# Performance work log

Hardware: AMD Instinct MI355X
Metric: run time of the kernel (lower is better)

Reference implementation:

```python
import jax, jax.numpy as jnp
import numpy as np

N, E = 100000, 1600000
FEATS, HIDDEN, CLASSES, DEPTH = 512, 64, 16, 10
EMB_DIM = 1 + int(np.log2(HIDDEN))   # 7
ADJ_H = 4 + EMB_DIM                  # 11
DIFF = 0.9


def setup_inputs() -> dict:
    key = jax.random.key(0)
    ks = jax.random.split(key, 8)
    return {
        "x": jax.random.normal(ks[0], (N, FEATS), jnp.float32),
        "edges": jax.random.randint(ks[1], (2, E), 0, N, jnp.int32),
        "W_dim": jax.random.normal(ks[2], (FEATS, HIDDEN), jnp.float32) / np.sqrt(FEATS),
        "b_dim": jnp.zeros((HIDDEN,), jnp.float32),
        "emb": jax.random.normal(ks[3], (HIDDEN, EMB_DIM), jnp.float32),
        "W_a1": jax.random.normal(ks[4], (2 + EMB_DIM, ADJ_H), jnp.float32) / np.sqrt(2 + EMB_DIM),
        "b_a1": jnp.zeros((ADJ_H,), jnp.float32),
        "W_a2": jax.random.normal(ks[5], (ADJ_H, 1), jnp.float32) / np.sqrt(ADJ_H),
        "b_a2": jnp.zeros((1,), jnp.float32),
        "W_cls": jax.random.normal(ks[6], (HIDDEN, CLASSES), jnp.float32) / np.sqrt(HIDDEN),
        "b_cls": jnp.zeros((CLASSES,), jnp.float32),
    }


def reference(x, edges, W_dim, b_dim, emb, W_a1, b_a1, W_a2, b_a2, W_cls, b_cls):
    n = x.shape[0]
    src, dst = edges[0], edges[1]
    # symmetric-normalized sparse aggregation (GCN-style GraphConv, cached norm)
    deg = jax.ops.segment_sum(jnp.ones(src.shape[0], x.dtype), dst, num_segments=n)
    dinv = jnp.where(deg > 0, jax.lax.rsqrt(jnp.maximum(deg, 1.0)), 0.0)
    wnorm = dinv[src] * dinv[dst]  # [E]

    def conv(h):  # [n, H] -> [n, H]
        return jax.ops.segment_sum(h[src] * wnorm[:, None], dst, num_segments=n)

    h = x @ W_dim + b_dim        # [n, HIDDEN]
    h0 = h
    for _ in range(DEPTH):       # personalized-PageRank-style diffusion
        h = conv(h) * DIFF + (1.0 - DIFF) * h0

    hdim = h.shape[1]
    xt = h.T.reshape(-1, 1)      # [HIDDEN*n, 1]
    h0t = h0.T.reshape(-1, 1)
    # class_indicator built after reshape(-1,1): num_classes = 1 -> all-zero indices
    e = jnp.broadcast_to(emb[0], (xt.shape[0], emb.shape[1]))  # [HIDDEN*n, EMB_DIM]
    f = jnp.concatenate([xt, h0t, e], axis=1)                  # [HIDDEN*n, 9]
    f = jax.nn.leaky_relu(f @ W_a1 + b_a1, negative_slope=0.01)
    f = (f @ W_a2 + b_a2) * 0.5                                # [HIDDEN*n, 1]
    h = f.reshape(hdim, n).T                                   # [n, HIDDEN]
    # dropout: eval mode -> no-op
    h0 = h
    for _ in range(DEPTH):
        h = conv(h) * DIFF + (1.0 - DIFF) * h0
    return h @ W_cls + b_cls     # [n, CLASSES]
```

## Files before the change

kernel.cpp:

```cpp
#include <hip/hip_runtime.h>
#include <hip/hip_bf16.h>
#include <hip/hip_fp16.h>
#include <stdint.h>

#define FEATS   512
#define HIDDEN  64
#define CLASSES 16
#define EMB_DIM 7
#define ADJ_H   11
#define DEPTH   10

typedef __hip_bfloat16 bf16;
typedef __attribute__((ext_vector_type(8))) short short8;
typedef __attribute__((ext_vector_type(4))) float f32x4;

__device__ __forceinline__ float b2f(bf16 v) { return __bfloat162float(v); }

__global__ void k_detect(const unsigned short* __restrict__ xs, int* __restrict__ flag) {
    __shared__ int cnt;
    if (threadIdx.x == 0) cnt = 0;
    __syncthreads();
    int c = 0;
    for (int i = threadIdx.x; i < 4096; i += 256) {
        unsigned e = (xs[i] >> 7) & 0xFFu;
        if (e >= 134u) c++;
    }
    atomicAdd(&cnt, c);
    __syncthreads();
    if (threadIdx.x == 0) *flag = (cnt < 64) ? 1 : 0;
}

__global__ __launch_bounds__(256) void k_deg(const int* __restrict__ edges,
                                             int* __restrict__ deg, int E) {
    int e = blockIdx.x * 256 + threadIdx.x;
    if (e < E) atomicAdd(&deg[edges[E + e]], 1);
}

__global__ __launch_bounds__(256) void k_scan1(const int* __restrict__ deg,
                                               int* __restrict__ offs,
                                               int* __restrict__ bsum, int n) {
    __shared__ int ts[256];
    int t = threadIdx.x;
    int base = blockIdx.x * 1024 + t * 4;
    int v0 = (base + 0 < n) ? deg[base + 0] : 0;
    int v1 = (base + 1 < n) ? deg[base + 1] : 0;
    int v2 = (base + 2 < n) ? deg[base + 2] : 0;
    int v3 = (base + 3 < n) ? deg[base + 3] : 0;
    int tsum = v0 + v1 + v2 + v3;
    ts[t] = tsum;
    __syncthreads();
    for (int d = 1; d < 256; d <<= 1) {
        int add = (t >= d) ? ts[t - d] : 0;
        __syncthreads();
        ts[t] += add;
        __syncthreads();
    }
    int excl = ts[t] - tsum;
    if (base + 0 < n) offs[base + 0] = excl;
    if (base + 1 < n) offs[base + 1] = excl + v0;
    if (base + 2 < n) offs[base + 2] = excl + v0 + v1;
    if (base + 3 < n) offs[base + 3] = excl + v0 + v1 + v2;
    if (t == 255) bsum[blockIdx.x] = ts[255];
}

__global__ void k_scan2(const int* __restrict__ bsum, int* __restrict__ bpref,
                        int* __restrict__ offs, int nb, int n) {
    if (threadIdx.x == 0 && blockIdx.x == 0) {
        int run = 0;
        for (int i = 0; i < nb; ++i) { bpref[i] = run; run += bsum[i]; }
        offs[n] = run;
    }
}

__global__ __launch_bounds__(256) void k_scan3(int* __restrict__ offs,
                                               const int* __restrict__ bpref, int n) {
    int i = blockIdx.x * 256 + threadIdx.x;
    if (i < n) offs[i] += bpref[i >> 10];
}

__global__ __launch_bounds__(256) void k_fill(const int* __restrict__ edges,
                                              const int* __restrict__ offs,
                                              int* __restrict__ cursor,
                                              const int* __restrict__ deg,
                                              unsigned* __restrict__ ew, int E) {
    int e = blockIdx.x * 256 + threadIdx.x;
    if (e < E) {
        int src = edges[e];
        int dst = edges[E + e];
        int pos = offs[dst] + atomicAdd(&cursor[dst], 1);
        int ds = deg[src], dd = deg[dst];
        float w = (ds > 0 ? rsqrtf((float)ds) : 0.f) * (dd > 0 ? rsqrtf((float)dd) : 0.f);
        int w15 = (int)(w * 16384.0f + 0.5f);
        if (w15 > 32767) w15 = 32767;
        ew[pos] = ((unsigned)src << 15) | (unsigned)w15;
    }
}

__global__ void k_mlpconst(const void* __restrict__ emb, const void* __restrict__ W_a1,
                           const void* __restrict__ b_a1, const void* __restrict__ W_a2,
                           const void* __restrict__ b_a2, const int* __restrict__ flag,
                           float* __restrict__ C) {
    int isbf = *flag;
    auto g = [&](const void* p, int i) -> float {
        return isbf ? b2f(((const bf16*)p)[i]) : ((const float*)p)[i];
    };
    int j = threadIdx.x;
    if (j < ADJ_H) {
        float c = g(b_a1, j);
        for (int k = 0; k < EMB_DIM; ++k)
            c += g(emb, k) * g(W_a1, (2 + k) * ADJ_H + j);
        C[j]      = c;
        C[11 + j] = g(W_a1, 0 * ADJ_H + j);
        C[22 + j] = g(W_a1, 1 * ADJ_H + j);
        C[33 + j] = g(W_a2, j);
    }
    if (j == 0) C[44] = g(b_a2, 0);
}

__global__ __launch_bounds__(256) void k_gemm_mfma(const void* __restrict__ xraw,
                                                   const int* __restrict__ flag,
                                                   const void* __restrict__ Wraw,
                                                   const void* __restrict__ braw,
                                                   __half* __restrict__ out, int n) {
    __shared__ short Wt[64 * 520];
    int t = threadIdx.x;
    int isbf = *flag;
    if (isbf) {
        const unsigned short* wr = (const unsigned short*)Wraw;
        for (int e = t; e < FEATS * HIDDEN; e += 256)
            Wt[(e & 63) * 520 + (e >> 6)] = (short)wr[e];
    } else {
        const float* wr = (const float*)Wraw;
        for (int e = t; e < FEATS * HIDDEN; e += 256)
            Wt[(e & 63) * 520 + (e >> 6)] = (short)(__float_as_uint(wr[e]) >> 16);
    }
    __syncthreads();

    int wv = t >> 6;
    int lane = t & 63;
    int quad = lane >> 4, l16 = lane & 15;
    int rowbase = blockIdx.x * 256 + wv * 64;

    f32x4 acc[4][4];
    #pragma unroll
    for (int a = 0; a < 4; ++a)
        #pragma unroll
        for (int b = 0; b < 4; ++b)
            acc[a][b] = (f32x4){0.f, 0.f, 0.f, 0.f};

    if (isbf) {
        const short* x = (const short*)xraw;
        for (int ks = 0; ks < 16; ++ks) {
            short8 bfr[4];
            #pragma unroll
            for (int nt = 0; nt < 4; ++nt)
                bfr[nt] = *(const short8*)&Wt[(nt * 16 + l16) * 520 + ks * 32 + quad * 8];
            #pragma unroll
            for (int rt = 0; rt < 4; ++rt) {
                int arow = rowbase + rt * 16 + l16;
                if (arow >= n) arow = n - 1;
                short8 a = *(const short8*)(x + (size_t)arow * FEATS + ks * 32 + quad * 8);
                #pragma unroll
                for (int nt = 0; nt < 4; ++nt)
                    acc[rt][nt] = __builtin_amdgcn_mfma_f32_16x16x32_bf16(a, bfr[nt], acc[rt][nt], 0, 0, 0);
            }
        }
    } else {
        const float* x = (const float*)xraw;
        for (int ks = 0; ks < 16; ++ks) {
            short8 bfr[4];
            #pragma unroll
            for (int nt = 0; nt < 4; ++nt)
                bfr[nt] = *(const short8*)&Wt[(nt * 16 + l16) * 520 + ks * 32 + quad * 8];
            #pragma unroll
            for (int rt = 0; rt < 4; ++rt) {
                int arow = rowbase + rt * 16 + l16;
                if (arow >= n) arow = n - 1;
                const float* ap = x + (size_t)arow * FEATS + ks * 32 + quad * 8;
                short8 a;
                #pragma unroll
                for (int j = 0; j < 8; ++j)
                    a[j] = (short)(__float_as_uint(ap[j]) >> 16);
                #pragma unroll
                for (int nt = 0; nt < 4; ++nt)
                    acc[rt][nt] = __builtin_amdgcn_mfma_f32_16x16x32_bf16(a, bfr[nt], acc[rt][nt], 0, 0, 0);
            }
        }
    }

    float bias[4];
    #pragma unroll
    for (int nt = 0; nt < 4; ++nt)
        bias[nt] = isbf ? b2f(((const bf16*)braw)[nt * 16 + l16])
                        : ((const float*)braw)[nt * 16 + l16];

    #pragma unroll
    for (int rt = 0; rt < 4; ++rt)
        #pragma unroll
        for (int nt = 0; nt < 4; ++nt) {
            #pragma unroll
            for (int r = 0; r < 4; ++r) {
                int grow = rowbase + rt * 16 + quad * 4 + r;
                if (grow < n)
                    out[(size_t)grow * HIDDEN + nt * 16 + l16] =
                        __float2half(acc[rt][nt][r] + bias[nt]);
            }
        }
}

__global__ __launch_bounds__(256) void k_conv(const int* __restrict__ offs,
                                              const unsigned* __restrict__ ew,
                                              const __half* __restrict__ hin,
                                              const __half* __restrict__ h0,
                                              __half* __restrict__ hout, int n) {
    int wv = (blockIdx.x * 256 + threadIdx.x) >> 6;
    int nA = wv * 2;
    if (nA >= n) return;
    int nB = nA + 1;
    bool hasB = (nB < n);
    int lane = threadIdx.x & 63;
    int eg = lane >> 3;
    int li = lane & 7;
    int sA = offs[nA], eA = offs[nA + 1];
    int sB = hasB ? offs[nB] : 0;
    int eB = hasB ? offs[nB + 1] : 0;

    float4 a0 = make_float4(0.f,0.f,0.f,0.f), a1 = make_float4(0.f,0.f,0.f,0.f);
    float4 b0 = make_float4(0.f,0.f,0.f,0.f), b1 = make_float4(0.f,0.f,0.f,0.f);

    int pA = sA + eg, pB = sB + eg;
    while (pA < eA || pB < eB) {
        bool vA = pA < eA, vB = pB < eB;
        unsigned uA = 0, uB = 0;
        uint4 rA = make_uint4(0,0,0,0), rB = make_uint4(0,0,0,0);
        if (vA) {
            uA = ew[pA];
            rA = *(const uint4*)(hin + (size_t)(uA >> 15) * HIDDEN + li * 8);
        }
        if (vB) {
            uB = ew[pB];
            rB = *(const uint4*)(hin + (size_t)(uB >> 15) * HIDDEN + li * 8);
        }
        if (vA) {
            float w = (float)(uA & 0x7FFFu) * (1.0f / 16384.0f);
            float2 f0 = __half22float2(*(__half2*)&rA.x);
            float2 f1 = __half22float2(*(__half2*)&rA.y);
            float2 f2 = __half22float2(*(__half2*)&rA.z);
            float2 f3 = __half22float2(*(__half2*)&rA.w);
            a0.x += w*f0.x; a0.y += w*f0.y; a0.z += w*f1.x; a0.w += w*f1.y;
            a1.x += w*f2.x; a1.y += w*f2.y; a1.z += w*f3.x; a1.w += w*f3.y;
            pA += 8;
        }
        if (vB) {
            float w = (float)(uB & 0x7FFFu) * (1.0f / 16384.0f);
            float2 f0 = __half22float2(*(__half2*)&rB.x);
            float2 f1 = __half22float2(*(__half2*)&rB.y);
            float2 f2 = __half22float2(*(__half2*)&rB.z);
            float2 f3 = __half22float2(*(__half2*)&rB.w);
            b0.x += w*f0.x; b0.y += w*f0.y; b0.z += w*f1.x; b0.w += w*f1.y;
            b1.x += w*f2.x; b1.y += w*f2.y; b1.z += w*f3.x; b1.w += w*f3.y;
            pB += 8;
        }
    }

    #pragma unroll
    for (int d = 8; d <= 32; d <<= 1) {
        a0.x += __shfl_xor(a0.x, d); a0.y += __shfl_xor(a0.y, d);
        a0.z += __shfl_xor(a0.z, d); a0.w += __shfl_xor(a0.w, d);
        a1.x += __shfl_xor(a1.x, d); a1.y += __shfl_xor(a1.y, d);
        a1.z += __shfl_xor(a1.z, d); a1.w += __shfl_xor(a1.w, d);
        b0.x += __shfl_xor(b0.x, d); b0.y += __shfl_xor(b0.y, d);
        b0.z += __shfl_xor(b0.z, d); b0.w += __shfl_xor(b0.w, d);
        b1.x += __shfl_xor(b1.x, d); b1.y += __shfl_xor(b1.y, d);
        b1.z += __shfl_xor(b1.z, d); b1.w += __shfl_xor(b1.w, d);
    }

    if (eg < 2 && (eg == 0 || hasB)) {
        int node = (eg == 0) ? nA : nB;
        float4 c0 = (eg == 0) ? a0 : b0;
        float4 c1 = (eg == 0) ? a1 : b1;
        size_t o = (size_t)node * HIDDEN + li * 8;
        uint4 hv = *(const uint4*)(h0 + o);
        float2 g0 = __half22float2(*(__half2*)&hv.x);
        float2 g1 = __half22float2(*(__half2*)&hv.y);
        float2 g2 = __half22float2(*(__half2*)&hv.z);
        float2 g3 = __half22float2(*(__half2*)&hv.w);
        __half2 o0 = __floats2half2_rn(0.9f*c0.x + 0.1f*g0.x, 0.9f*c0.y + 0.1f*g0.y);
        __half2 o1 = __floats2half2_rn(0.9f*c0.z + 0.1f*g1.x, 0.9f*c0.w + 0.1f*g1.y);
        __half2 o2 = __floats2half2_rn(0.9f*c1.x + 0.1f*g2.x, 0.9f*c1.y + 0.1f*g2.y);
        __half2 o3 = __floats2half2_rn(0.9f*c1.z + 0.1f*g3.x, 0.9f*c1.w + 0.1f*g3.y);
        uint4 ov;
        ov.x = *(unsigned*)&o0; ov.y = *(unsigned*)&o1;
        ov.z = *(unsigned*)&o2; ov.w = *(unsigned*)&o3;
        *(uint4*)(hout + o) = ov;
    }
}

__global__ __launch_bounds__(256) void k_mlp(__half* __restrict__ h0io,
                                             const __half* __restrict__ hc,
                                             const float* __restrict__ C, int total2) {
    int i = blockIdx.x * 256 + threadIdx.x;
    if (i >= total2) return;
    float2 hv  = __half22float2(((const __half2*)hc)[i]);
    float2 h0v = __half22float2(((const __half2*)h0io)[i]);
    float sx = C[44], sy = C[44];
    #pragma unroll
    for (int j = 0; j < ADJ_H; ++j) {
        float bj = C[j], wh = C[11 + j], w0 = C[22 + j], wo = C[33 + j];
        float zx = bj + hv.x * wh + h0v.x * w0;
        float zy = bj + hv.y * wh + h0v.y * w0;
        zx = (zx > 0.f) ? zx : 0.01f * zx;
        zy = (zy > 0.f) ? zy : 0.01f * zy;
        sx += zx * wo;
        sy += zy * wo;
    }
    ((__half2*)h0io)[i] = __floats2half2_rn(0.5f * sx, 0.5f * sy);
}

__global__ __launch_bounds__(256) void k_cls(const __half* __restrict__ h,
                                             const void* __restrict__ Wcraw,
                                             const void* __restrict__ bcraw,
                                             void* __restrict__ outraw,
                                             const int* __restrict__ flag, int n) {
    __shared__ float hs[64][65];
    __shared__ float ws[64 * 16];
    __shared__ float bs[16];
    int t = threadIdx.x;
    int base = blockIdx.x * 64;
    int isbf = *flag;
    for (int it = 0; it < 16; ++it) {
        int e = it * 256 + t;
        int rr = e >> 6, cc = e & 63;
        int g = base + rr;
        hs[rr][cc] = (g < n) ? __half2float(h[(size_t)g * HIDDEN + cc]) : 0.f;
    }
    for (int it = 0; it < 4; ++it) {
        int e = it * 256 + t;
        ws[e] = isbf ? b2f(((const bf16*)Wcraw)[e]) : ((const float*)Wcraw)[e];
    }
    if (t < 16) bs[t] = isbf ? b2f(((const bf16*)bcraw)[t]) : ((const float*)bcraw)[t];
    __syncthreads();
    for (int q = 0; q < 4; ++q) {
        int e = q * 256 + t;
        int node = e >> 4, cls = e & 15;
        float acc = bs[cls];
        #pragma unroll 8
        for (int k = 0; k < HIDDEN; ++k)
            acc += hs[node][k] * ws[k * 16 + cls];
        int g = base + node;
        if (g < n) {
            size_t oi = (size_t)g * CLASSES + cls;
            if (isbf) ((bf16*)outraw)[oi] = __float2bfloat16(acc);
            else      ((float*)outraw)[oi] = acc;
        }
    }
}

extern "C" void kernel_launch(void* const* d_in, const int* in_sizes, int n_in,
                              void* d_out, int out_size, void* d_ws, size_t ws_size,
                              hipStream_t stream) {
    const void* x     = d_in[0];
    const int*  edges = (const int*)d_in[1];
    const void* W_dim = d_in[2];
    const void* b_dim = d_in[3];
    const void* emb   = d_in[4];
    const void* W_a1  = d_in[5];
    const void* b_a1  = d_in[6];
    const void* W_a2  = d_in[7];
    const void* b_a2  = d_in[8];
    const void* Wcls  = d_in[9];
    const void* bcls  = d_in[10];

    const int n = in_sizes[0] / FEATS;
    const int E = in_sizes[1] / 2;

    char* w = (char*)d_ws;
    size_t off = 0;
    auto alloc = [&](size_t bytes) -> void* {
        void* p = w + off;
        off = (off + bytes + 255) & ~(size_t)255;
        return p;
    };
    int*      deg    = (int*)     alloc((size_t)n * 4);
    int*      cursor = (int*)     alloc((size_t)n * 4);
    int*      offs   = (int*)     alloc((size_t)(n + 1) * 4);
    int*      bsum   = (int*)     alloc(4096 * 4);
    int*      bpref  = (int*)     alloc(4096 * 4);
    unsigned* ew     = (unsigned*)alloc((size_t)E * 4);
    float*    consts = (float*)   alloc(64 * 4);
    int*      flag   = (int*)     alloc(256);
    __half*   buf0   = (__half*)  alloc((size_t)n * HIDDEN * 2);
    __half*   bufA   = (__half*)  alloc((size_t)n * HIDDEN * 2);
    __half*   bufB   = (__half*)  alloc((size_t)n * HIDDEN * 2);

    int gE = (E + 255) / 256;
    int gN = (n + 255) / 256;
    int nb = (n + 1023) / 1024;
    int gConv = (n + 7) / 8;

    hipMemsetAsync(deg, 0, ((char*)cursor - (char*)deg) + (size_t)n * 4, stream);

    k_detect<<<1, 256, 0, stream>>>((const unsigned short*)x, flag);

    k_deg  <<<gE, 256, 0, stream>>>(edges, deg, E);
    k_scan1<<<nb, 256, 0, stream>>>(deg, offs, bsum, n);
    k_scan2<<<1, 64, 0, stream>>>(bsum, bpref, offs, nb, n);
    k_scan3<<<gN, 256, 0, stream>>>(offs, bpref, n);
    k_fill <<<gE, 256, 0, stream>>>(edges, offs, cursor, deg, ew, E);

    k_mlpconst<<<1, 64, 0, stream>>>(emb, W_a1, b_a1, W_a2, b_a2, flag, consts);

    k_gemm_mfma<<<(n + 255) / 256, 256, 0, stream>>>(x, flag, W_dim, b_dim, buf0, n);

    const __half* hin = buf0;
    for (int i = 0; i < DEPTH; ++i) {
        __half* ho = (i & 1) ? bufB : bufA;
        k_conv<<<gConv, 256, 0, stream>>>(offs, ew, hin, buf0, ho, n);
        hin = ho;
    }
    k_mlp<<<(n * (HIDDEN / 2) + 255) / 256, 256, 0, stream>>>(buf0, hin, consts, n * (HIDDEN / 2));

    hin = buf0;
    for (int i = 0; i < DEPTH; ++i) {
        __half* ho = (i & 1) ? bufB : bufA;
        k_conv<<<gConv, 256, 0, stream>>>(offs, ew, hin, buf0, ho, n);
        hin = ho;
    }
    k_cls<<<(n + 63) / 64, 256, 0, stream>>>(hin, Wcls, bcls, d_out, flag, n);
}
```

Baseline: 1.300 ms.

## Map one wavefront per node with one lane per feature in conv

Restructures the sparse aggregation kernel. The old version had each wave handle two nodes, with 8 edge groups doing 16-byte row gathers and a shuffle reduction. The new version has each wave handle one node, each lane owning one hidden feature, and loops over all of that node's edges sequentially, unrolled by 4 with scalar edge loads. This removes the cross-lane shuffle reduction and the two-node divergence. In exchange it issues 2-byte gathers per lane and serialises the edge loop within a wave, which may lengthen latency chains; the grid doubles accordingly.

```diff
diff --git a/kernel.cpp b/kernel.cpp
--- a/kernel.cpp
+++ b/kernel.cpp
@@ -213,87 +213,34 @@
                                               const __half* __restrict__ hin,
                                               const __half* __restrict__ h0,
                                               __half* __restrict__ hout, int n) {
-    int wv = (blockIdx.x * 256 + threadIdx.x) >> 6;
-    int nA = wv * 2;
-    if (nA >= n) return;
-    int nB = nA + 1;
-    bool hasB = (nB < n);
+    int node = __builtin_amdgcn_readfirstlane(blockIdx.x * 4 + ((int)threadIdx.x >> 6));
+    if (node >= n) return;
     int lane = threadIdx.x & 63;
-    int eg = lane >> 3;
-    int li = lane & 7;
-    int sA = offs[nA], eA = offs[nA + 1];
-    int sB = hasB ? offs[nB] : 0;
-    int eB = hasB ? offs[nB + 1] : 0;
-
-    float4 a0 = make_float4(0.f,0.f,0.f,0.f), a1 = make_float4(0.f,0.f,0.f,0.f);
-    float4 b0 = make_float4(0.f,0.f,0.f,0.f), b1 = make_float4(0.f,0.f,0.f,0.f);
-
-    int pA = sA + eg, pB = sB + eg;
-    while (pA < eA || pB < eB) {
-        bool vA = pA < eA, vB = pB < eB;
-        unsigned uA = 0, uB = 0;
-        uint4 rA = make_uint4(0,0,0,0), rB = make_uint4(0,0,0,0);
-        if (vA) {
-            uA = ew[pA];
-            rA = *(const uint4*)(hin + (size_t)(uA >> 15) * HIDDEN + li * 8);
-        }
-        if (vB) {
-            uB = ew[pB];
-            rB = *(const uint4*)(hin + (size_t)(uB >> 15) * HIDDEN + li * 8);
-        }
-        if (vA) {
-            float w = (float)(uA & 0x7FFFu) * (1.0f / 16384.0f);
-            float2 f0 = __half22float2(*(__half2*)&rA.x);
-            float2 f1 = __half22float2(*(__half2*)&rA.y);
-            float2 f2 = __half22float2(*(__half2*)&rA.z);
-            float2 f3 = __half22float2(*(__half2*)&rA.w);
-            a0.x += w*f0.x; a0.y += w*f0.y; a0.z += w*f1.x; a0.w += w*f1.y;
-            a1.x += w*f2.x; a1.y += w*f2.y; a1.z += w*f3.x; a1.w += w*f3.y;
-            pA += 8;
-        }
-        if (vB) {
-            float w = (float)(uB & 0x7FFFu) * (1.0f / 16384.0f);
-            float2 f0 = __half22float2(*(__half2*)&rB.x);
-            float2 f1 = __half22float2(*(__half2*)&rB.y);
-            float2 f2 = __half22float2(*(__half2*)&rB.z);
-            float2 f3 = __half22float2(*(__half2*)&rB.w);
-            b0.x += w*f0.x; b0.y += w*f0.y; b0.z += w*f1.x; b0.w += w*f1.y;
-            b1.x += w*f2.x; b1.y += w*f2.y; b1.z += w*f3.x; b1.w += w*f3.y;
-            pB += 8;
-        }
-    }
-
-    #pragma unroll
-    for (int d = 8; d <= 32; d <<= 1) {
-        a0.x += __shfl_xor(a0.x, d); a0.y += __shfl_xor(a0.y, d);
-        a0.z += __shfl_xor(a0.z, d); a0.w += __shfl_xor(a0.w, d);
-        a1.x += __shfl_xor(a1.x, d); a1.y += __shfl_xor(a1.y, d);
-        a1.z += __shfl_xor(a1.z, d); a1.w += __shfl_xor(a1.w, d);
-        b0.x += __shfl_xor(b0.x, d); b0.y += __shfl_xor(b0.y, d);
-        b0.z += __shfl_xor(b0.z, d); b0.w += __shfl_xor(b0.w, d);
-        b1.x += __shfl_xor(b1.x, d); b1.y += __shfl_xor(b1.y, d);
-        b1.z += __shfl_xor(b1.z, d); b1.w += __shfl_xor(b1.w, d);
-    }
-
-    if (eg < 2 && (eg == 0 || hasB)) {
-        int node = (eg == 0) ? nA : nB;
-        float4 c0 = (eg == 0) ? a0 : b0;
-        float4 c1 = (eg == 0) ? a1 : b1;
-        size_t o = (size_t)node * HIDDEN + li * 8;
-        uint4 hv = *(const uint4*)(h0 + o);
-        float2 g0 = __half22float2(*(__half2*)&hv.x);
-        float2 g1 = __half22float2(*(__half2*)&hv.y);
-        float2 g2 = __half22float2(*(__half2*)&hv.z);
-        float2 g3 = __half22float2(*(__half2*)&hv.w);
-        __half2 o0 = __floats2half2_rn(0.9f*c0.x + 0.1f*g0.x, 0.9f*c0.y + 0.1f*g0.y);
-        __half2 o1 = __floats2half2_rn(0.9f*c0.z + 0.1f*g1.x, 0.9f*c0.w + 0.1f*g1.y);
-        __half2 o2 = __floats2half2_rn(0.9f*c1.x + 0.1f*g2.x, 0.9f*c1.y + 0.1f*g2.y);
-        __half2 o3 = __floats2half2_rn(0.9f*c1.z + 0.1f*g3.x, 0.9f*c1.w + 0.1f*g3.y);
-        uint4 ov;
-        ov.x = *(unsigned*)&o0; ov.y = *(unsigned*)&o1;
-        ov.z = *(unsigned*)&o2; ov.w = *(unsigned*)&o3;
-        *(uint4*)(hout + o) = ov;
-    }
+    int start = offs[node];
+    int end   = offs[node + 1];
+    float acc0 = 0.f, acc1 = 0.f;
+    int p = start;
+    for (; p + 4 <= end; p += 4) {
+        unsigned u0 = ew[p + 0];
+        unsigned u1 = ew[p + 1];
+        unsigned u2 = ew[p + 2];
+        unsigned u3 = ew[p + 3];
+        float v0 = __half2float(hin[(size_t)(u0 >> 15) * HIDDEN + lane]);
+        float v1 = __half2float(hin[(size_t)(u1 >> 15) * HIDDEN + lane]);
+        float v2 = __half2float(hin[(size_t)(u2 >> 15) * HIDDEN + lane]);
+        float v3 = __half2float(hin[(size_t)(u3 >> 15) * HIDDEN + lane]);
+        acc0 += (float)(u0 & 0x7FFFu) * v0;
+        acc1 += (float)(u1 & 0x7FFFu) * v1;
+        acc0 += (float)(u2 & 0x7FFFu) * v2;
+        acc1 += (float)(u3 & 0x7FFFu) * v3;
+    }
+    for (; p < end; ++p) {
+        unsigned u = ew[p];
+        acc0 += (float)(u & 0x7FFFu) * __half2float(hin[(size_t)(u >> 15) * HIDDEN + lane]);
+    }
+    float acc = (acc0 + acc1) * (1.0f / 16384.0f);
+    float h0v = __half2float(h0[(size_t)node * HIDDEN + lane]);
+    hout[(size_t)node * HIDDEN + lane] = __float2half(0.9f * acc + 0.1f * h0v);
 }
 
 __global__ __launch_bounds__(256) void k_mlp(__half* __restrict__ h0io,
@@ -396,7 +343,7 @@
     int gE = (E + 255) / 256;
     int gN = (n + 255) / 256;
     int nb = (n + 1023) / 1024;
-    int gConv = (n + 7) / 8;
+    int gConv = (n + 3) / 4;
 
     hipMemsetAsync(deg, 0, ((char*)cursor - (char*)deg) + (size_t)n * 4, stream);
 
```

New measurement: 1.471 ms. 13.1% more time.
